# Optimization experiments

Measured on AMD Instinct MI355X. Metric: run time of the kernel, lower is better.

The kernel has to match this reference:

```python
import jax, jax.numpy as jnp
import numpy as np

B, C, H, W = 2, 128, 96, 96
HEADS, DHEAD, WIN = 4, 32, 5
INNER = HEADS * DHEAD
PAD = WIN // 2


def setup_inputs() -> dict:
    key = jax.random.key(0)
    k1, k2, k3, k4, k5 = jax.random.split(key, 5)
    s = 1.0 / np.sqrt(C)
    return {
        "x": jax.random.normal(k1, (B, C, H, W), dtype=jnp.float32),
        "wq": jax.random.normal(k2, (INNER, C), dtype=jnp.float32) * s,
        "wk": jax.random.normal(k3, (INNER, C), dtype=jnp.float32) * s,
        "wv": jax.random.normal(k4, (INNER, C), dtype=jnp.float32) * s,
        "wproj": jax.random.normal(k5, (C, INNER), dtype=jnp.float32) * s,
    }


def _windows(t):
    # same neighborhood ordering as F.unfold (row-major over kernel offsets).
    tp = jnp.pad(t, ((0, 0), (0, 0), (0, 0), (PAD, PAD), (PAD, PAD)))
    wins = [tp[:, :, :, di:di + H, dj:dj + W]
            for di in range(WIN) for dj in range(WIN)]
    return jnp.stack(wins, axis=3)


def reference(x, wq, wk, wv, wproj):
    # 1x1 convs == per-pixel linear maps
    q = jnp.einsum('oc,bcxy->boxy', wq, x).reshape(B, HEADS, DHEAD, H, W)
    k = jnp.einsum('oc,bcxy->boxy', wk, x).reshape(B, HEADS, DHEAD, H, W)
    v = jnp.einsum('oc,bcxy->boxy', wv, x).reshape(B, HEADS, DHEAD, H, W)

    k_win = _windows(k)  # (B,h,d,25,H,W)
    v_win = _windows(v)

    scale = 1.0 / np.sqrt(DHEAD)
    attn = jnp.einsum('bhdxy,bhdkxy->bhkxy', q, k_win) * scale
    attn = jax.nn.softmax(attn, axis=2)  # softmax over the 25 window positions
    out = jnp.einsum('bhkxy,bhdkxy->bhdxy', attn, v_win)

    out = out.reshape(B, INNER, H, W)
    return jnp.einsum('co,boxy->bcxy', wproj, out)
```

## Files before the change

kernel.cpp:

```cpp
#include <hip/hip_runtime.h>
#include <hip/hip_fp16.h>

#define PP 9216

typedef _Float16 f16x8 __attribute__((ext_vector_type(8)));
typedef _Float16 f16x4 __attribute__((ext_vector_type(4)));
typedef _Float16 h2    __attribute__((ext_vector_type(2)));
typedef float    f32x4 __attribute__((ext_vector_type(4)));

#define SXW 136
#define SSW 68
#define SPW 72
#define SVW 72

#define OFF_X    0
#define OFF_K    17408
#define OFF_Q    35840
#define OFF_INV  40192
#define LDS_BYTES 40448

__global__ __launch_bounds__(256) void prep_w(
    const float* __restrict__ wq, const float* __restrict__ wk,
    const float* __restrict__ wv, const float* __restrict__ wp,
    _Float16* __restrict__ wqkv16, _Float16* __restrict__ wp16)
{
    int e = (blockIdx.x * 256 + threadIdx.x) * 4;
    const float* src;
    _Float16* dst;
    if (e < 49152) {
        int o = e >> 7;
        src = (o < 128) ? (wq + (size_t)o * 128)
            : (o < 256) ? (wk + (size_t)(o - 128) * 128)
                        : (wv + (size_t)(o - 256) * 128);
        src += (e & 127);
        dst = wqkv16 + e;
    } else {
        int j = e - 49152;
        src = wp + j;
        dst = wp16 + j;
    }
    float4 v = *(const float4*)src;
    f16x4 h;
    h[0] = (_Float16)v.x; h[1] = (_Float16)v.y;
    h[2] = (_Float16)v.z; h[3] = (_Float16)v.w;
    *(f16x4*)dst = h;
}

__global__ __launch_bounds__(256, 4) void fused_attn(
    const float* __restrict__ x, const _Float16* __restrict__ wqkv,
    const _Float16* __restrict__ wp16, float* __restrict__ out)
{
    __shared__ __align__(16) char smem[LDS_BYTES];
    _Float16* sX  = (_Float16*)(smem + OFF_X);
    _Float16* sK  = (_Float16*)(smem + OFF_K);
    _Float16* sQ  = (_Float16*)(smem + OFF_Q);
    _Float16* sAo = (_Float16*)(smem + OFF_Q);
    float*    sInv= (float*)(smem + OFF_INV);

    const int t = threadIdx.x;
    const int w = t >> 6, lane = t & 63, lm = lane & 15, quad = lane >> 4;

    const int wgid = (blockIdx.x & 7) * 144 + (blockIdx.x >> 3);
    const int b = wgid / 576;
    const int rem = wgid - b * 576;
    const int x0 = (rem % 24) * 4, y0 = (rem / 24) * 4;

    const float* xb = x + (size_t)b * 128 * PP;
    float* ob = out + (size_t)b * 128 * PP;

    #pragma unroll
    for (int i = 0; i < 16; i++) {
        int c   = i * 8 + (t >> 5);
        int pos = (t & 31) * 2;
        int gy = y0 - 2 + (pos >> 3);
        int gx = x0 - 2 + (pos & 7);
        float2 v = make_float2(0.f, 0.f);
        if ((unsigned)gy < 96u && (unsigned)gx < 96u)
            v = *(const float2*)(xb + (size_t)c * PP + gy * 96 + gx);
        sX[pos * SXW + c]       = (_Float16)v.x;
        sX[(pos + 1) * SXW + c] = (_Float16)v.y;
    }
    __syncthreads();

    h2 vpk[2][4][2];
    #pragma unroll
    for (int m = 0; m < 4; m++) {
        f16x8 A[4];
        #pragma unroll
        for (int kc = 0; kc < 4; kc++)
            A[kc] = *(const f16x8*)(sX + (m * 16 + lm) * SXW + kc * 32 + quad * 8);
        #pragma unroll
        for (int ni = 0; ni < 2; ni++) {
            int n = w + 4 * ni;
            const _Float16* wr = wqkv + (size_t)(128 + n * 16 + lm) * 128;
            f32x4 acc = {0.f, 0.f, 0.f, 0.f};
            #pragma unroll
            for (int kc = 0; kc < 4; kc++)
                acc = __builtin_amdgcn_mfma_f32_16x16x32_f16(
                    A[kc], *(const f16x8*)(wr + kc * 32 + quad * 8), acc, 0, 0, 0);
            #pragma unroll
            for (int r = 0; r < 4; r++)
                sK[(m * 16 + quad * 4 + r) * SXW + n * 16 + lm] = (_Float16)acc[r];
        }
        #pragma unroll
        for (int nn = 0; nn < 2; nn++) {
            const _Float16* wr = wqkv + (size_t)(256 + (2 * w + nn) * 16 + lm) * 128;
            f32x4 acc = {0.f, 0.f, 0.f, 0.f};
            #pragma unroll
            for (int kc = 0; kc < 4; kc++)
                acc = __builtin_amdgcn_mfma_f32_16x16x32_f16(
                    A[kc], *(const f16x8*)(wr + kc * 32 + quad * 8), acc, 0, 0, 0);
            vpk[nn][m][0][0] = (_Float16)acc[0]; vpk[nn][m][0][1] = (_Float16)acc[1];
            vpk[nn][m][1][0] = (_Float16)acc[2]; vpk[nn][m][1][1] = (_Float16)acc[3];
        }
    }

    {
        int hrow = ((lm >> 2) + 2) * 8 + (lm & 3) + 2;
        f16x8 A[4];
        #pragma unroll
        for (int kc = 0; kc < 4; kc++)
            A[kc] = *(const f16x8*)(sX + hrow * SXW + kc * 32 + quad * 8);
        #pragma unroll
        for (int nn = 0; nn < 2; nn++) {
            const _Float16* wr = wqkv + (size_t)((2 * w + nn) * 16 + lm) * 128;
            f32x4 acc = {0.f, 0.f, 0.f, 0.f};
            #pragma unroll
            for (int kc = 0; kc < 4; kc++)
                acc = __builtin_amdgcn_mfma_f32_16x16x32_f16(
                    A[kc], *(const f16x8*)(wr + kc * 32 + quad * 8), acc, 0, 0, 0);
            #pragma unroll
            for (int r = 0; r < 4; r++)
                sQ[(quad * 4 + r) * SXW + (2 * w + nn) * 16 + lm] = (_Float16)acc[r];
        }
    }
    __syncthreads();

    float*    sSh = (float*)(smem + OFF_X + w * 4352);
    _Float16* sPh = (_Float16*)(smem + OFF_X + w * 4352);

    {
        f16x8 Aq = *(const f16x8*)(sQ + lm * SXW + w * 32 + quad * 8);
        #pragma unroll
        for (int n = 0; n < 4; n++) {
            f16x8 Bk = *(const f16x8*)(sK + (n * 16 + lm) * SXW + w * 32 + quad * 8);
            f32x4 acc = {0.f, 0.f, 0.f, 0.f};
            acc = __builtin_amdgcn_mfma_f32_16x16x32_f16(Aq, Bk, acc, 0, 0, 0);
            #pragma unroll
            for (int r = 0; r < 4; r++)
                sSh[(quad * 4 + r) * SSW + n * 16 + lm] = acc[r];
        }
    }

    {
        const int spx = lane >> 2, sub = lane & 3;
        const int py = spx >> 2, pxx = spx & 3;
        float sv[16];
        #pragma unroll
        for (int j4 = 0; j4 < 4; j4++)
            *(float4*)(sv + j4 * 4) = *(const float4*)(sSh + spx * SSW + sub * 16 + j4 * 4);
        const float scale = 0.17677669529663689f;
        float sj[16];
        float mx = -1e30f;
        #pragma unroll
        for (int j = 0; j < 16; j++) {
            int pos = sub * 16 + j;
            int hy = pos >> 3, hx = pos & 7;
            bool memb = (hy >= py) & (hy < py + 5) & (hx >= pxx) & (hx < pxx + 5);
            sj[j] = memb ? sv[j] * scale : -1e30f;
            mx = fmaxf(mx, sj[j]);
        }
        mx = fmaxf(mx, __shfl_xor(mx, 1));
        mx = fmaxf(mx, __shfl_xor(mx, 2));
        float sum = 0.f;
        f16x8 ev0, ev1;
        #pragma unroll
        for (int j = 0; j < 16; j++) {
            float e = __expf(sj[j] - mx);
            sum += e;
            if (j < 8) ev0[j] = (_Float16)e; else ev1[j - 8] = (_Float16)e;
        }
        sum += __shfl_xor(sum, 1);
        sum += __shfl_xor(sum, 2);
        *(f16x8*)(sPh + spx * SPW + sub * 16)     = ev0;
        *(f16x8*)(sPh + spx * SPW + sub * 16 + 8) = ev1;
        if (sub == 0) sInv[w * 16 + spx] = 1.f / sum;
    }
    __syncthreads();

    _Float16* sVh = (_Float16*)(smem + OFF_K + w * 4608);
    #pragma unroll
    for (int nn = 0; nn < 2; nn++)
        #pragma unroll
        for (int m = 0; m < 4; m++)
            #pragma unroll
            for (int rp = 0; rp < 2; rp++)
                *(h2*)(sVh + (nn * 16 + lm) * SVW + m * 16 + quad * 4 + rp * 2)
                    = vpk[nn][m][rp];

    {
        f16x8 Ap[2];
        #pragma unroll
        for (int kc = 0; kc < 2; kc++)
            Ap[kc] = *(const f16x8*)(sPh + lm * SPW + kc * 32 + quad * 8);
        float ivr[4];
        *(float4*)ivr = *(const float4*)(sInv + w * 16 + quad * 4);
        #pragma unroll
        for (int nd = 0; nd < 2; nd++) {
            f32x4 acc = {0.f, 0.f, 0.f, 0.f};
            #pragma unroll
            for (int kc = 0; kc < 2; kc++) {
                f16x8 Bv = *(const f16x8*)(sVh + (nd * 16 + lm) * SVW + kc * 32 + quad * 8);
                acc = __builtin_amdgcn_mfma_f32_16x16x32_f16(Ap[kc], Bv, acc, 0, 0, 0);
            }
            #pragma unroll
            for (int r = 0; r < 4; r++)
                sAo[(quad * 4 + r) * SXW + w * 32 + nd * 16 + lm] =
                    (_Float16)(acc[r] * ivr[r]);
        }
    }
    __syncthreads();

    {
        f16x8 Bf[4];
        #pragma unroll
        for (int kc = 0; kc < 4; kc++)
            Bf[kc] = *(const f16x8*)(sAo + lm * SXW + kc * 32 + quad * 8);
        int gp = (y0 + (lm >> 2)) * 96 + x0 + (lm & 3);
        #pragma unroll
        for (int mi = 0; mi < 2; mi++) {
            const _Float16* wr = wp16 + (size_t)((w * 2 + mi) * 16 + lm) * 128;
            f32x4 acc = {0.f, 0.f, 0.f, 0.f};
            #pragma unroll
            for (int kc = 0; kc < 4; kc++)
                acc = __builtin_amdgcn_mfma_f32_16x16x32_f16(
                    *(const f16x8*)(wr + kc * 32 + quad * 8), Bf[kc], acc, 0, 0, 0);
            int c0 = (w * 2 + mi) * 16 + quad * 4;
            #pragma unroll
            for (int r = 0; r < 4; r++)
                ob[(size_t)(c0 + r) * PP + gp] = acc[r];
        }
    }
}

extern "C" void kernel_launch(void* const* d_in, const int* in_sizes, int n_in,
                              void* d_out, int out_size, void* d_ws, size_t ws_size,
                              hipStream_t stream)
{
    const float* x  = (const float*)d_in[0];
    const float* wq = (const float*)d_in[1];
    const float* wk = (const float*)d_in[2];
    const float* wv = (const float*)d_in[3];
    const float* wp = (const float*)d_in[4];
    float* out = (float*)d_out;

    _Float16* wqkv16 = (_Float16*)d_ws;
    _Float16* wp16   = wqkv16 + 49152;

    prep_w<<<dim3(64), 256, 0, stream>>>(wq, wk, wv, wp, wqkv16, wp16);
    fused_attn<<<dim3(1152), 256, 0, stream>>>(x, wqkv16, wp16, out);
}
```

Baseline: 107.9 us.

## Shrink LDS with XOR swizzle, keep scores in registers, raise occupancy

Replaces padded LDS rows with XOR-swizzled unpadded layouts and reuses one buffer for Q and the attention output, cutting LDS from about 40 KB to 32 KB. Launch bounds go from 4 to 5 workgroups per CU. The softmax now runs directly on the MFMA accumulator registers using 16-lane shuffles, which removes the fp32 score round-trip through LDS. The x loads are batched into registers before the LDS stores, and the K and V projections are merged into one loop. The risks are more register pressure under the tighter launch bound and extra shuffle work in the softmax.

```diff
diff --git a/kernel.cpp b/kernel.cpp
--- a/kernel.cpp
+++ b/kernel.cpp
@@ -8,16 +8,14 @@
 typedef _Float16 h2    __attribute__((ext_vector_type(2)));
 typedef float    f32x4 __attribute__((ext_vector_type(4)));
 
-#define SXW 136
-#define SSW 68
-#define SPW 72
-#define SVW 72
-
-#define OFF_X    0
-#define OFF_K    17408
-#define OFF_Q    35840
-#define OFF_INV  40192
-#define LDS_BYTES 40448
+#define LDS_BYTES 32768
+
+__device__ __forceinline__ int swz128(int row, int hc) {
+    return row * 128 + (((hc >> 3) ^ (row & 15)) << 3) + (hc & 7);
+}
+__device__ __forceinline__ int swz64(int row, int hc) {
+    return row * 64 + (((hc >> 3) ^ (row & 7)) << 3) + (hc & 7);
+}
 
 __global__ __launch_bounds__(256) void prep_w(
     const float* __restrict__ wq, const float* __restrict__ wk,
@@ -46,16 +44,13 @@
     *(f16x4*)dst = h;
 }
 
-__global__ __launch_bounds__(256, 4) void fused_attn(
+__global__ __launch_bounds__(256, 5) void fused_attn(
     const float* __restrict__ x, const _Float16* __restrict__ wqkv,
     const _Float16* __restrict__ wp16, float* __restrict__ out)
 {
     __shared__ __align__(16) char smem[LDS_BYTES];
-    _Float16* sX  = (_Float16*)(smem + OFF_X);
-    _Float16* sK  = (_Float16*)(smem + OFF_K);
-    _Float16* sQ  = (_Float16*)(smem + OFF_Q);
-    _Float16* sAo = (_Float16*)(smem + OFF_Q);
-    float*    sInv= (float*)(smem + OFF_INV);
+    _Float16* sA = (_Float16*)smem;
+    _Float16* sB = (_Float16*)(smem + 16384);
 
     const int t = threadIdx.x;
     const int w = t >> 6, lane = t & 63, lm = lane & 15, quad = lane >> 4;
@@ -68,17 +63,23 @@
     const float* xb = x + (size_t)b * 128 * PP;
     float* ob = out + (size_t)b * 128 * PP;
 
-    #pragma unroll
-    for (int i = 0; i < 16; i++) {
-        int c   = i * 8 + (t >> 5);
-        int pos = (t & 31) * 2;
-        int gy = y0 - 2 + (pos >> 3);
-        int gx = x0 - 2 + (pos & 7);
-        float2 v = make_float2(0.f, 0.f);
-        if ((unsigned)gy < 96u && (unsigned)gx < 96u)
-            v = *(const float2*)(xb + (size_t)c * PP + gy * 96 + gx);
-        sX[pos * SXW + c]       = (_Float16)v.x;
-        sX[(pos + 1) * SXW + c] = (_Float16)v.y;
+    {
+        const int pos = (t & 31) * 2;
+        const int gy = y0 - 2 + (pos >> 3);
+        const int gx = x0 - 2 + (pos & 7);
+        const bool inb = ((unsigned)gy < 96u) && ((unsigned)gx < 96u);
+        const float* src = xb + (size_t)(t >> 5) * PP + gy * 96 + gx;
+        float2 vv[16];
+        #pragma unroll
+        for (int i = 0; i < 16; i++)
+            vv[i] = inb ? *(const float2*)(src + (size_t)(i * 8) * PP)
+                        : make_float2(0.f, 0.f);
+        #pragma unroll
+        for (int i = 0; i < 16; i++) {
+            int c = i * 8 + (t >> 5);
+            sA[swz128(pos,     c)] = (_Float16)vv[i].x;
+            sA[swz128(pos + 1, c)] = (_Float16)vv[i].y;
+        }
     }
     __syncthreads();
 
@@ -88,135 +89,132 @@
         f16x8 A[4];
         #pragma unroll
         for (int kc = 0; kc < 4; kc++)
-            A[kc] = *(const f16x8*)(sX + (m * 16 + lm) * SXW + kc * 32 + quad * 8);
-        #pragma unroll
-        for (int ni = 0; ni < 2; ni++) {
-            int n = w + 4 * ni;
-            const _Float16* wr = wqkv + (size_t)(128 + n * 16 + lm) * 128;
+            A[kc] = *(const f16x8*)(sA + swz128(m * 16 + lm, kc * 32 + quad * 8));
+        #pragma unroll
+        for (int ni = 0; ni < 4; ni++) {
+            const int wrow = (ni < 2) ? (128 + (w + 4 * ni) * 16 + lm)
+                                      : (256 + (2 * w + (ni - 2)) * 16 + lm);
+            const _Float16* wr = wqkv + (size_t)wrow * 128;
             f32x4 acc = {0.f, 0.f, 0.f, 0.f};
             #pragma unroll
             for (int kc = 0; kc < 4; kc++)
                 acc = __builtin_amdgcn_mfma_f32_16x16x32_f16(
                     A[kc], *(const f16x8*)(wr + kc * 32 + quad * 8), acc, 0, 0, 0);
-            #pragma unroll
-            for (int r = 0; r < 4; r++)
-                sK[(m * 16 + quad * 4 + r) * SXW + n * 16 + lm] = (_Float16)acc[r];
-        }
-        #pragma unroll
-        for (int nn = 0; nn < 2; nn++) {
-            const _Float16* wr = wqkv + (size_t)(256 + (2 * w + nn) * 16 + lm) * 128;
-            f32x4 acc = {0.f, 0.f, 0.f, 0.f};
-            #pragma unroll
-            for (int kc = 0; kc < 4; kc++)
-                acc = __builtin_amdgcn_mfma_f32_16x16x32_f16(
-                    A[kc], *(const f16x8*)(wr + kc * 32 + quad * 8), acc, 0, 0, 0);
-            vpk[nn][m][0][0] = (_Float16)acc[0]; vpk[nn][m][0][1] = (_Float16)acc[1];
-            vpk[nn][m][1][0] = (_Float16)acc[2]; vpk[nn][m][1][1] = (_Float16)acc[3];
-        }
-    }
-
+            if (ni < 2) {
+                int n = w + 4 * ni;
+                #pragma unroll
+                for (int r = 0; r < 4; r++)
+                    sB[swz128(m * 16 + quad * 4 + r, n * 16 + lm)] = (_Float16)acc[r];
+            } else {
+                h2 p0, p1;
+                p0[0] = (_Float16)acc[0]; p0[1] = (_Float16)acc[1];
+                p1[0] = (_Float16)acc[2]; p1[1] = (_Float16)acc[3];
+                vpk[ni - 2][m][0] = p0;
+                vpk[ni - 2][m][1] = p1;
+            }
+        }
+    }
+
+    f16x8 A3[4];
     {
         int hrow = ((lm >> 2) + 2) * 8 + (lm & 3) + 2;
-        f16x8 A[4];
-        #pragma unroll
-        for (int kc = 0; kc < 4; kc++)
-            A[kc] = *(const f16x8*)(sX + hrow * SXW + kc * 32 + quad * 8);
-        #pragma unroll
-        for (int nn = 0; nn < 2; nn++) {
-            const _Float16* wr = wqkv + (size_t)((2 * w + nn) * 16 + lm) * 128;
-            f32x4 acc = {0.f, 0.f, 0.f, 0.f};
-            #pragma unroll
-            for (int kc = 0; kc < 4; kc++)
-                acc = __builtin_amdgcn_mfma_f32_16x16x32_f16(
-                    A[kc], *(const f16x8*)(wr + kc * 32 + quad * 8), acc, 0, 0, 0);
-            #pragma unroll
-            for (int r = 0; r < 4; r++)
-                sQ[(quad * 4 + r) * SXW + (2 * w + nn) * 16 + lm] = (_Float16)acc[r];
-        }
-    }
-    __syncthreads();
-
-    float*    sSh = (float*)(smem + OFF_X + w * 4352);
-    _Float16* sPh = (_Float16*)(smem + OFF_X + w * 4352);
-
-    {
-        f16x8 Aq = *(const f16x8*)(sQ + lm * SXW + w * 32 + quad * 8);
+        #pragma unroll
+        for (int kc = 0; kc < 4; kc++)
+            A3[kc] = *(const f16x8*)(sA + swz128(hrow, kc * 32 + quad * 8));
+    }
+    __syncthreads();
+
+    _Float16* sQ = sA + 4608;
+    #pragma unroll
+    for (int nn = 0; nn < 2; nn++) {
+        const _Float16* wr = wqkv + (size_t)((2 * w + nn) * 16 + lm) * 128;
+        f32x4 acc = {0.f, 0.f, 0.f, 0.f};
+        #pragma unroll
+        for (int kc = 0; kc < 4; kc++)
+            acc = __builtin_amdgcn_mfma_f32_16x16x32_f16(
+                A3[kc], *(const f16x8*)(wr + kc * 32 + quad * 8), acc, 0, 0, 0);
+        #pragma unroll
+        for (int r = 0; r < 4; r++)
+            sQ[swz128(quad * 4 + r, (2 * w + nn) * 16 + lm)] = (_Float16)acc[r];
+    }
+
+    f32x4 S[4];
+    {
+        f16x8 Aq = *(const f16x8*)(sQ + swz128(lm, w * 32 + quad * 8));
         #pragma unroll
         for (int n = 0; n < 4; n++) {
-            f16x8 Bk = *(const f16x8*)(sK + (n * 16 + lm) * SXW + w * 32 + quad * 8);
-            f32x4 acc = {0.f, 0.f, 0.f, 0.f};
-            acc = __builtin_amdgcn_mfma_f32_16x16x32_f16(Aq, Bk, acc, 0, 0, 0);
-            #pragma unroll
-            for (int r = 0; r < 4; r++)
-                sSh[(quad * 4 + r) * SSW + n * 16 + lm] = acc[r];
-        }
-    }
-
-    {
-        const int spx = lane >> 2, sub = lane & 3;
-        const int py = spx >> 2, pxx = spx & 3;
-        float sv[16];
-        #pragma unroll
-        for (int j4 = 0; j4 < 4; j4++)
-            *(float4*)(sv + j4 * 4) = *(const float4*)(sSh + spx * SSW + sub * 16 + j4 * 4);
+            f16x8 Bk = *(const f16x8*)(sB + swz128(n * 16 + lm, w * 32 + quad * 8));
+            f32x4 z = {0.f, 0.f, 0.f, 0.f};
+            S[n] = __builtin_amdgcn_mfma_f32_16x16x32_f16(Aq, Bk, z, 0, 0, 0);
+        }
+    }
+
+    _Float16* sPh = sA + w * 1152;
+    float inv4[4];
+    {
         const float scale = 0.17677669529663689f;
-        float sj[16];
-        float mx = -1e30f;
-        #pragma unroll
-        for (int j = 0; j < 16; j++) {
-            int pos = sub * 16 + j;
-            int hy = pos >> 3, hx = pos & 7;
-            bool memb = (hy >= py) & (hy < py + 5) & (hx >= pxx) & (hx < pxx + 5);
-            sj[j] = memb ? sv[j] * scale : -1e30f;
-            mx = fmaxf(mx, sj[j]);
-        }
-        mx = fmaxf(mx, __shfl_xor(mx, 1));
-        mx = fmaxf(mx, __shfl_xor(mx, 2));
-        float sum = 0.f;
-        f16x8 ev0, ev1;
-        #pragma unroll
-        for (int j = 0; j < 16; j++) {
-            float e = __expf(sj[j] - mx);
-            sum += e;
-            if (j < 8) ev0[j] = (_Float16)e; else ev1[j - 8] = (_Float16)e;
-        }
-        sum += __shfl_xor(sum, 1);
-        sum += __shfl_xor(sum, 2);
-        *(f16x8*)(sPh + spx * SPW + sub * 16)     = ev0;
-        *(f16x8*)(sPh + spx * SPW + sub * 16 + 8) = ev1;
-        if (sub == 0) sInv[w * 16 + spx] = 1.f / sum;
-    }
-    __syncthreads();
-
-    _Float16* sVh = (_Float16*)(smem + OFF_K + w * 4608);
+        #pragma unroll
+        for (int r = 0; r < 4; r++) {
+            float e[4];
+            float mx = -1e30f;
+            #pragma unroll
+            for (int n = 0; n < 4; n++) {
+                int hy = n * 2 + (lm >> 3), hx = lm & 7;
+                bool memb = (hy >= quad) && (hy < quad + 5) && (hx >= r) && (hx < r + 5);
+                e[n] = memb ? S[n][r] * scale : -1e30f;
+                mx = fmaxf(mx, e[n]);
+            }
+            mx = fmaxf(mx, __shfl_xor(mx, 1));
+            mx = fmaxf(mx, __shfl_xor(mx, 2));
+            mx = fmaxf(mx, __shfl_xor(mx, 4));
+            mx = fmaxf(mx, __shfl_xor(mx, 8));
+            float sum = 0.f;
+            #pragma unroll
+            for (int n = 0; n < 4; n++) {
+                float ev = __expf(e[n] - mx);
+                e[n] = ev;
+                sum += ev;
+            }
+            sum += __shfl_xor(sum, 1);
+            sum += __shfl_xor(sum, 2);
+            sum += __shfl_xor(sum, 4);
+            sum += __shfl_xor(sum, 8);
+            inv4[r] = 1.f / sum;
+            #pragma unroll
+            for (int n = 0; n < 4; n++)
+                sPh[(quad * 4 + r) * 72 + n * 16 + lm] = (_Float16)e[n];
+        }
+    }
+    __syncthreads();
+
+    _Float16* sVh = sB + w * 2048;
     #pragma unroll
     for (int nn = 0; nn < 2; nn++)
         #pragma unroll
         for (int m = 0; m < 4; m++)
             #pragma unroll
             for (int rp = 0; rp < 2; rp++)
-                *(h2*)(sVh + (nn * 16 + lm) * SVW + m * 16 + quad * 4 + rp * 2)
+                *(h2*)(sVh + swz64(nn * 16 + lm, m * 16 + quad * 4 + rp * 2))
                     = vpk[nn][m][rp];
 
+    _Float16* sAo = sQ;
     {
         f16x8 Ap[2];
         #pragma unroll
         for (int kc = 0; kc < 2; kc++)
-            Ap[kc] = *(const f16x8*)(sPh + lm * SPW + kc * 32 + quad * 8);
-        float ivr[4];
-        *(float4*)ivr = *(const float4*)(sInv + w * 16 + quad * 4);
+            Ap[kc] = *(const f16x8*)(sPh + lm * 72 + kc * 32 + quad * 8);
         #pragma unroll
         for (int nd = 0; nd < 2; nd++) {
             f32x4 acc = {0.f, 0.f, 0.f, 0.f};
             #pragma unroll
             for (int kc = 0; kc < 2; kc++) {
-                f16x8 Bv = *(const f16x8*)(sVh + (nd * 16 + lm) * SVW + kc * 32 + quad * 8);
+                f16x8 Bv = *(const f16x8*)(sVh + swz64(nd * 16 + lm, kc * 32 + quad * 8));
                 acc = __builtin_amdgcn_mfma_f32_16x16x32_f16(Ap[kc], Bv, acc, 0, 0, 0);
             }
             #pragma unroll
             for (int r = 0; r < 4; r++)
-                sAo[(quad * 4 + r) * SXW + w * 32 + nd * 16 + lm] =
-                    (_Float16)(acc[r] * ivr[r]);
+                sAo[swz128(quad * 4 + r, w * 32 + nd * 16 + lm)] =
+                    (_Float16)(acc[r] * inv4[r]);
         }
     }
     __syncthreads();
@@ -225,7 +223,7 @@
         f16x8 Bf[4];
         #pragma unroll
         for (int kc = 0; kc < 4; kc++)
-            Bf[kc] = *(const f16x8*)(sAo + lm * SXW + kc * 32 + quad * 8);
+            Bf[kc] = *(const f16x8*)(sAo + swz128(lm, kc * 32 + quad * 8));
         int gp = (y0 + (lm >> 2)) * 96 + x0 + (lm & 3);
         #pragma unroll
         for (int mi = 0; mi < 2; mi++) {
```

Result: slower. 125.8 us (+16.7%).
